# Kernel tuning notes

Measured on AMD Instinct MI355X. Metric: run time of the kernel, lower is better.

Reference implementation:

```python
import jax, jax.numpy as jnp
import numpy as np

B = 2048          # batch
K = 32            # max active features per side
NF = 22528        # feature_set.num_features
L1 = 2048
L2 = 16
L3 = 32
P = 8             # num_psqt_buckets
NLS = 8           # num_ls_buckets
QP = 255.0        # 8-bit unsigned LSQ upper bound


def setup_inputs() -> dict:
    key = jax.random.key(0)
    ks = jax.random.split(key, 16)
    us = jax.random.bernoulli(ks[0], 0.5, (B, 1)).astype(jnp.float32)
    them = 1.0 - us
    white_indices = jax.random.randint(ks[1], (B, K), 0, NF)
    black_indices = jax.random.randint(ks[2], (B, K), 0, NF)
    white_values = jnp.ones((B, K), jnp.float32)
    black_values = jnp.ones((B, K), jnp.float32)
    psqt_indices = jax.random.randint(ks[3], (B,), 0, P)
    layer_stack_indices = jax.random.randint(ks[4], (B,), 0, NLS)
    # parameters
    ft_weight = jax.random.normal(ks[5], (NF, L1 + P), jnp.float32) * 0.01
    ft_bias = jax.random.normal(ks[6], (L1 + P,), jnp.float32) * 0.01
    lsq_s = jnp.full((4,), 1.0 / 128.0, jnp.float32)  # per-group step size
    W1 = jax.random.normal(ks[7], (NLS, L2, L1), jnp.float32) * (1.0 / np.sqrt(L1))
    b1 = jnp.zeros((NLS, L2), jnp.float32)
    W2 = jax.random.normal(ks[8], (NLS, L3, L2), jnp.float32) * (1.0 / np.sqrt(L2))
    b2 = jnp.zeros((NLS, L3), jnp.float32)
    Wo = jax.random.normal(ks[9], (NLS, 1, L3), jnp.float32) * (1.0 / np.sqrt(L3))
    bo = jnp.zeros((NLS, 1), jnp.float32)
    return dict(us=us, them=them, white_indices=white_indices, white_values=white_values,
                black_indices=black_indices, black_values=black_values,
                psqt_indices=psqt_indices, layer_stack_indices=layer_stack_indices,
                ft_weight=ft_weight, ft_bias=ft_bias, lsq_s=lsq_s,
                W1=W1, b1=b1, W2=W2, b2=b2, Wo=Wo, bo=bo)


def _feature_transform(idx, val, ft_weight, ft_bias):
    # sparse accumulation: sum_k val[b,k] * ft_weight[idx[b,k], :]
    emb = ft_weight[idx]                           # [B, K, L1+P]
    return jnp.einsum('bk,bkd->bd', val, emb) + ft_bias


def _lsq(x, s):
    # LSQ activation, 4 groups over feature dim, 8-bit unsigned, STE round
    b, d = x.shape
    g = x.reshape(b, 4, d // 4) / s[None, :, None]
    gc = jnp.clip(g, 0.0, QP)
    gq = gc + jax.lax.stop_gradient(jnp.round(gc) - gc)
    return (gq * s[None, :, None]).reshape(b, d)


def reference(us, them, white_indices, white_values, black_indices, black_values,
              psqt_indices, layer_stack_indices,
              ft_weight, ft_bias, lsq_s, W1, b1, W2, b2, Wo, bo):
    wp = _feature_transform(white_indices, white_values, ft_weight, ft_bias)
    bp = _feature_transform(black_indices, black_values, ft_weight, ft_bias)
    w, wpsqt = wp[:, :L1], wp[:, L1:]
    b, bpsqt = bp[:, :L1], bp[:, L1:]
    l0 = us * jnp.concatenate([w, b], axis=1) + them * jnp.concatenate([b, w], axis=1)
    l0q = _lsq(l0, lsq_s)                          # [B, 2*L1]
    s0, s1, s2, s3 = jnp.split(l0q, 4, axis=1)
    l0_mixed = jnp.concatenate([s0 * s1, s2 * s3], axis=1)   # [B, L1]
    # psqt bucket gather
    wps = jnp.take_along_axis(wpsqt, psqt_indices[:, None], axis=1)  # [B,1]
    bps = jnp.take_along_axis(bpsqt, psqt_indices[:, None], axis=1)
    # per-sample layer-stack (expert) selection
    i = layer_stack_indices
    h1 = jnp.clip(jnp.einsum('bi,boi->bo', l0_mixed, W1[i]) + b1[i], 0.0, 1.0)
    h2 = jnp.clip(jnp.einsum('bi,boi->bo', h1, W2[i]) + b2[i], 0.0, 1.0)
    ls_out = jnp.einsum('bi,boi->bo', h2, Wo[i]) + bo[i]     # [B,1]
    return ls_out + (wps - bps) * (us - 0.5)
```

## Files before the change

kernel.cpp:

```cpp
#include <hip/hip_runtime.h>

#define BB 2048
#define K 32
#define ROW 2056
#define L1D 2048
#define NFEAT 22528

typedef unsigned short us8 __attribute__((ext_vector_type(8)));
typedef float f8 __attribute__((ext_vector_type(8)));

#define TBLC_BYTES ((size_t)NFEAT * 2048 * 2)
#define W1_ELEMS   ((size_t)8 * 16 * L1D)
#define W1_OFF     TBLC_BYTES
#define WS_NEEDED  (TBLC_BYTES + W1_ELEMS * 2)

#define TBL_N8 (NFEAT * 256)
#define W1_N8  (W1_ELEMS / 8)

__device__ __forceinline__ float bf2f(unsigned short s) {
    union { unsigned int u; float f; } v; v.u = ((unsigned int)s) << 16; return v.f;
}

__device__ __forceinline__ unsigned short f2bf(float f) {
    union { float f; unsigned int u; } v; v.f = f;
    const unsigned int u = v.u;
    return (unsigned short)((u + 0x7fffu + ((u >> 16) & 1u)) >> 16);
}

__device__ __forceinline__ void fma4(float4& a, float v, const float4 t) {
    a.x = fmaf(v, t.x, a.x); a.y = fmaf(v, t.y, a.y);
    a.z = fmaf(v, t.z, a.z); a.w = fmaf(v, t.w, a.w);
}

__device__ __forceinline__ float4 add4(float4 a, float4 b) {
    float4 r; r.x = a.x + b.x; r.y = a.y + b.y; r.z = a.z + b.z; r.w = a.w + b.w;
    return r;
}

__device__ __forceinline__ float4 mix4(float ua, float4 a, float ub, float4 b) {
    float4 r;
    r.x = fmaf(ua, a.x, ub * b.x); r.y = fmaf(ua, a.y, ub * b.y);
    r.z = fmaf(ua, a.z, ub * b.z); r.w = fmaf(ua, a.w, ub * b.w);
    return r;
}

__device__ __forceinline__ float lsq1(float g, float s) {
    return rintf(fminf(fmaxf(g / s, 0.f), 255.f)) * s;
}

__device__ __forceinline__ float4 lsq4(float4 g, float s) {
    float4 r;
    r.x = lsq1(g.x, s); r.y = lsq1(g.y, s); r.z = lsq1(g.z, s); r.w = lsq1(g.w, s);
    return r;
}

__device__ __forceinline__ float4 mul4(float4 a, float4 b) {
    float4 r; r.x = a.x * b.x; r.y = a.y * b.y; r.z = a.z * b.z; r.w = a.w * b.w;
    return r;
}

__global__ __launch_bounds__(256) void conv_all(const float* __restrict__ ftw,
                                                const float* __restrict__ W1,
                                                unsigned short* __restrict__ tblc,
                                                unsigned short* __restrict__ w1bf) {
    int i = blockIdx.x * 256 + threadIdx.x;
    const int stride = gridDim.x * 256;
    for (; i < TBL_N8 + W1_N8; i += stride) {
        const float* src;
        unsigned short* dst;
        if (i < TBL_N8) {
            const int row = i >> 8, c = i & 255;
            src = ftw + (size_t)row * ROW + c * 8;
            dst = tblc + ((size_t)row << 11) + c * 8;
        } else {
            const int j = i - TBL_N8;
            src = W1 + (size_t)j * 8;
            dst = w1bf + (size_t)j * 8;
        }
        const float4 a = ((const float4*)src)[0];
        const float4 b = ((const float4*)src)[1];
        us8 o;
        o[0] = f2bf(a.x); o[1] = f2bf(a.y); o[2] = f2bf(a.z); o[3] = f2bf(a.w);
        o[4] = f2bf(b.x); o[5] = f2bf(b.y); o[6] = f2bf(b.z); o[7] = f2bf(b.w);
        *(us8*)dst = o;
    }
}

__global__ __launch_bounds__(256, 8) void nnue_main(
    const float* __restrict__ us_p, const float* __restrict__ them_p,
    const int* __restrict__ widx, const float* __restrict__ wval,
    const int* __restrict__ bidx, const float* __restrict__ bval,
    const int* __restrict__ psqt_idx, const int* __restrict__ ls_idx,
    const float* __restrict__ ftw,
    const float* __restrict__ ftb, const float* __restrict__ lsq_s,
    const unsigned short* __restrict__ tblc,
    const unsigned short* __restrict__ w1bf,
    const float* __restrict__ b1, const float* __restrict__ W2,
    const float* __restrict__ b2, const float* __restrict__ Wo,
    const float* __restrict__ bo, float* __restrict__ out)
{
    const int b = blockIdx.x;
    const int t = threadIdx.x;

    __shared__ f8    sQA[256];
    __shared__ f8    sQB[256];
    __shared__ float sH1t[16];
    __shared__ float sH1[16];
    __shared__ float sH2[32];
    __shared__ float sPsq;

    const float usv = us_p[b];
    const float thv = them_p[b];

    f8 aw = (f8)0.f, ab = (f8)0.f;
    #pragma unroll 8
    for (int k = 0; k < K; ++k) {
        const int   iw = widx[b * K + k];
        const float vw = wval[b * K + k];
        const int   ib = bidx[b * K + k];
        const float vb = bval[b * K + k];
        const us8 lw = ((const us8*)(tblc + ((size_t)iw << 11)))[t];
        const us8 lb = ((const us8*)(tblc + ((size_t)ib << 11)))[t];
        #pragma unroll
        for (int j = 0; j < 8; ++j) aw[j] = fmaf(vw, bf2f(lw[j]), aw[j]);
        #pragma unroll
        for (int j = 0; j < 8; ++j) ab[j] = fmaf(vb, bf2f(lb[j]), ab[j]);
    }

    const int pi = psqt_idx[b];
    if (t < 64) {
        const int k = t & 31;
        const int   idx = (t < 32) ? widx[b * K + k] : bidx[b * K + k];
        const float val = (t < 32) ? wval[b * K + k] : bval[b * K + k];
        float c = val * ftw[(size_t)idx * ROW + 2048 + pi];
        c += __shfl_down(c, 16, 32); c += __shfl_down(c, 8, 32);
        c += __shfl_down(c, 4, 32);  c += __shfl_down(c, 2, 32);
        c += __shfl_down(c, 1, 32);
        const float bsum = __shfl(c, 32);
        if (t == 0) sPsq = (c - bsum) * (usv - 0.5f);
    }

    const float s0 = lsq_s[0], s1 = lsq_s[1], s2 = lsq_s[2], s3 = lsq_s[3];
    const float4 bl = ((const float4*)ftb)[2 * t];
    const float4 bh = ((const float4*)ftb)[2 * t + 1];
    float4 awl = {aw[0], aw[1], aw[2], aw[3]}, awh = {aw[4], aw[5], aw[6], aw[7]};
    float4 abl = {ab[0], ab[1], ab[2], ab[3]}, abh = {ab[4], ab[5], ab[6], ab[7]};
    awl = add4(awl, bl); awh = add4(awh, bh);
    abl = add4(abl, bl); abh = add4(abh, bh);
    const float sA = (t < 128) ? s0 : s1;
    const float sB = (t < 128) ? s2 : s3;
    const float4 qal = lsq4(mix4(usv, awl, thv, abl), sA);
    const float4 qah = lsq4(mix4(usv, awh, thv, abh), sA);
    const float4 qbl = lsq4(mix4(usv, abl, thv, awl), sB);
    const float4 qbh = lsq4(mix4(usv, abh, thv, awh), sB);
    f8 qa, qb;
    qa[0]=qal.x; qa[1]=qal.y; qa[2]=qal.z; qa[3]=qal.w;
    qa[4]=qah.x; qa[5]=qah.y; qa[6]=qah.z; qa[7]=qah.w;
    qb[0]=qbl.x; qb[1]=qbl.y; qb[2]=qbl.z; qb[3]=qbl.w;
    qb[4]=qbh.x; qb[5]=qbh.y; qb[6]=qbh.z; qb[7]=qbh.w;
    sQA[t] = qa;
    sQB[t] = qb;
    __syncthreads();

    if (t < 128) {
        const f8 m = sQA[t] * sQA[t + 128];
        sQA[t] = m;
    } else {
        const f8 m = sQB[t - 128] * sQB[t];
        sQB[t] = m;
    }
    __syncthreads();

    const int i = ls_idx[b];
    {
        const int o   = t >> 4;
        const int sub = t & 15;
        const us8* Wrow = (const us8*)(w1bf + (((size_t)i * 16 + o) << 11));
        f8 a8 = (f8)0.f;
        #pragma unroll
        for (int jj = 0; jj < 8; ++jj) {
            const int c = sub + (jj << 4);
            const f8 m = sQA[c];
            const us8 w = Wrow[c];
            #pragma unroll
            for (int j = 0; j < 8; ++j) a8[j] = fmaf(m[j], bf2f(w[j]), a8[j]);
        }
        #pragma unroll
        for (int jj = 8; jj < 16; ++jj) {
            const int c = sub + (jj << 4);
            const f8 m = sQB[c];
            const us8 w = Wrow[c];
            #pragma unroll
            for (int j = 0; j < 8; ++j) a8[j] = fmaf(m[j], bf2f(w[j]), a8[j]);
        }
        float acc = ((a8[0]+a8[1]) + (a8[2]+a8[3])) + ((a8[4]+a8[5]) + (a8[6]+a8[7]));
        acc += __shfl_down(acc, 8, 16); acc += __shfl_down(acc, 4, 16);
        acc += __shfl_down(acc, 2, 16); acc += __shfl_down(acc, 1, 16);
        if (sub == 0) sH1t[o] = acc;
    }
    __syncthreads();

    if (t < 16) {
        const float v = sH1t[t] + b1[i * 16 + t];
        sH1[t] = fminf(fmaxf(v, 0.f), 1.f);
    }
    __syncthreads();

    if (t < 32) {
        const float* W2i = W2 + (size_t)i * 32 * 16 + t * 16;
        float v = b2[i * 32 + t];
        #pragma unroll
        for (int j = 0; j < 16; ++j) v = fmaf(sH1[j], W2i[j], v);
        sH2[t] = fminf(fmaxf(v, 0.f), 1.f);
    }
    __syncthreads();

    if (t == 0) {
        const float* Woi = Wo + (size_t)i * 32;
        float v = bo[i];
        #pragma unroll
        for (int j = 0; j < 32; ++j) v = fmaf(sH2[j], Woi[j], v);
        out[b] = v + sPsq;
    }
}

__global__ __launch_bounds__(512, 8) void nnue_fwd_f32(
    const float* __restrict__ us_p, const float* __restrict__ them_p,
    const int* __restrict__ widx, const float* __restrict__ wval,
    const int* __restrict__ bidx, const float* __restrict__ bval,
    const int* __restrict__ psqt_idx, const int* __restrict__ ls_idx,
    const float* __restrict__ ftw, const float* __restrict__ ftb,
    const float* __restrict__ lsq_s, const float* __restrict__ W1,
    const float* __restrict__ b1, const float* __restrict__ W2,
    const float* __restrict__ b2, const float* __restrict__ Wo,
    const float* __restrict__ bo, float* __restrict__ out)
{
    const int b = blockIdx.x;
    const int t = threadIdx.x;
    __shared__ float4 sQA[512]; __shared__ float4 sQB[512]; __shared__ float4 sM[512];
    __shared__ float sH1t[16]; __shared__ float sH1[16]; __shared__ float sH2[32];
    __shared__ float sPsq;
    const float usv = us_p[b]; const float thv = them_p[b];
    float4 aw = {0,0,0,0}, ab = {0,0,0,0};
    #pragma unroll 4
    for (int k = 0; k < K; ++k) {
        const int iw = widx[b*K+k]; const float vw = wval[b*K+k];
        const int ib = bidx[b*K+k]; const float vb = bval[b*K+k];
        fma4(aw, vw, ((const float4*)(ftw + (size_t)iw * ROW))[t]);
        fma4(ab, vb, ((const float4*)(ftw + (size_t)ib * ROW))[t]);
    }
    const int pi = psqt_idx[b];
    if (t < 64) {
        const int k = t & 31;
        const int   idx = (t < 32) ? widx[b*K+k] : bidx[b*K+k];
        const float val = (t < 32) ? wval[b*K+k] : bval[b*K+k];
        float c = val * ftw[(size_t)idx * ROW + 2048 + pi];
        c += __shfl_down(c, 16, 32); c += __shfl_down(c, 8, 32);
        c += __shfl_down(c, 4, 32); c += __shfl_down(c, 2, 32); c += __shfl_down(c, 1, 32);
        const float bsum = __shfl(c, 32);
        if (t == 0) sPsq = (c - bsum) * (usv - 0.5f);
    }
    const float s0 = lsq_s[0], s1 = lsq_s[1], s2 = lsq_s[2], s3 = lsq_s[3];
    const float4 bias = ((const float4*)ftb)[t];
    aw = add4(aw, bias); ab = add4(ab, bias);
    const float sA = (t < 256) ? s0 : s1;
    const float sB = (t < 256) ? s2 : s3;
    sQA[t] = lsq4(mix4(usv, aw, thv, ab), sA);
    sQB[t] = lsq4(mix4(usv, ab, thv, aw), sB);
    __syncthreads();
    if (t < 256) { sM[t] = mul4(sQA[t], sQA[t+256]); sM[t+256] = mul4(sQB[t], sQB[t+256]); }
    __syncthreads();
    const int i = ls_idx[b];
    const float* W1i = W1 + (size_t)i * 16 * L1D;
    {
        const int o = t >> 5; const int sub = t & 31;
        const float4* Wrow = (const float4*)(W1i + o * L1D);
        float4 a4 = {0,0,0,0};
        #pragma unroll
        for (int jj = 0; jj < 16; ++jj) {
            const int j4 = sub + (jj << 5);
            const float4 m = sM[j4]; const float4 w = Wrow[j4];
            a4.x = fmaf(m.x, w.x, a4.x); a4.y = fmaf(m.y, w.y, a4.y);
            a4.z = fmaf(m.z, w.z, a4.z); a4.w = fmaf(m.w, w.w, a4.w);
        }
        float acc = (a4.x + a4.y) + (a4.z + a4.w);
        acc += __shfl_down(acc, 16, 32); acc += __shfl_down(acc, 8, 32);
        acc += __shfl_down(acc, 4, 32); acc += __shfl_down(acc, 2, 32); acc += __shfl_down(acc, 1, 32);
        if (sub == 0) sH1t[o] = acc;
    }
    __syncthreads();
    if (t < 16) sH1[t] = fminf(fmaxf(sH1t[t] + b1[i*16+t], 0.f), 1.f);
    __syncthreads();
    if (t < 32) {
        const float* W2i = W2 + (size_t)i * 32 * 16 + t * 16;
        float v = b2[i*32+t];
        #pragma unroll
        for (int j = 0; j < 16; ++j) v = fmaf(sH1[j], W2i[j], v);
        sH2[t] = fminf(fmaxf(v, 0.f), 1.f);
    }
    __syncthreads();
    if (t == 0) {
        const float* Woi = Wo + (size_t)i * 32;
        float v = bo[i];
        #pragma unroll
        for (int j = 0; j < 32; ++j) v = fmaf(sH2[j], Woi[j], v);
        out[b] = v + sPsq;
    }
}

extern "C" void kernel_launch(void* const* d_in, const int* in_sizes, int n_in,
                              void* d_out, int out_size, void* d_ws, size_t ws_size,
                              hipStream_t stream) {
    const float* us_p  = (const float*)d_in[0];
    const float* them  = (const float*)d_in[1];
    const int*   widx  = (const int*)d_in[2];
    const float* wval  = (const float*)d_in[3];
    const int*   bidx  = (const int*)d_in[4];
    const float* bval  = (const float*)d_in[5];
    const int*   pidx  = (const int*)d_in[6];
    const int*   lidx  = (const int*)d_in[7];
    const float* ftw   = (const float*)d_in[8];
    const float* ftb   = (const float*)d_in[9];
    const float* lsqs  = (const float*)d_in[10];
    const float* W1    = (const float*)d_in[11];
    const float* b1    = (const float*)d_in[12];
    const float* W2    = (const float*)d_in[13];
    const float* b2    = (const float*)d_in[14];
    const float* Wo    = (const float*)d_in[15];
    const float* bo    = (const float*)d_in[16];
    float* out = (float*)d_out;

    if (ws_size >= WS_NEEDED) {
        unsigned short* tblc = (unsigned short*)d_ws;
        unsigned short* w1bf = (unsigned short*)((char*)d_ws + W1_OFF);
        conv_all<<<dim3(8192), dim3(256), 0, stream>>>(ftw, W1, tblc, w1bf);
        nnue_main<<<dim3(BB), dim3(256), 0, stream>>>(
            us_p, them, widx, wval, bidx, bval, pidx, lidx,
            ftw, ftb, lsqs, tblc, w1bf, b1, W2, b2, Wo, bo, out);
    } else {
        nnue_fwd_f32<<<dim3(BB), dim3(512), 0, stream>>>(
            us_p, them, widx, wval, bidx, bval, pidx, lidx,
            ftw, ftb, lsqs, W1, b1, W2, b2, Wo, bo, out);
    }
}
```

Before: 378.6 us.

## Slice feature table into column blocks and split gather from layer stack

The bf16 feature table is re-laid out into 32 column slices of 64 values per row, so each gather block reads a small, cache-resident slice for a group of 32 samples. A new gather_mix kernel accumulates, applies bias and LSQ, forms the pairwise product and writes a bf16 mixed activation buffer G. A separate combine kernel then runs the layer stack from G. The aim is better L2 reuse of table rows across samples. The cost is an extra kernel launch, a round trip through global memory for G, and bf16 rounding of the mixed activations.

```diff
diff --git a/kernel.cpp b/kernel.cpp
--- a/kernel.cpp
+++ b/kernel.cpp
@@ -5,17 +5,20 @@
 #define ROW 2056
 #define L1D 2048
 #define NFEAT 22528
+#define NSL 32
 
 typedef unsigned short us8 __attribute__((ext_vector_type(8)));
 typedef float f8 __attribute__((ext_vector_type(8)));
 
-#define TBLC_BYTES ((size_t)NFEAT * 2048 * 2)
+#define TBL2_BYTES ((size_t)NSL * NFEAT * 64 * 2)
 #define W1_ELEMS   ((size_t)8 * 16 * L1D)
-#define W1_OFF     TBLC_BYTES
-#define WS_NEEDED  (TBLC_BYTES + W1_ELEMS * 2)
-
-#define TBL_N8 (NFEAT * 256)
-#define W1_N8  (W1_ELEMS / 8)
+#define W1_OFF     TBL2_BYTES
+#define G_OFF      (TBL2_BYTES + W1_ELEMS * 2)
+#define G_BYTES    ((size_t)BB * L1D * 2)
+#define WS_NEEDED  (G_OFF + G_BYTES)
+
+#define TBL2_N8 (NSL * NFEAT * 8)
+#define W1_N8   ((int)(W1_ELEMS / 8))
 
 __device__ __forceinline__ float bf2f(unsigned short s) {
     union { unsigned int u; float f; } v; v.u = ((unsigned int)s) << 16; return v.f;
@@ -61,39 +64,134 @@
 
 __global__ __launch_bounds__(256) void conv_all(const float* __restrict__ ftw,
                                                 const float* __restrict__ W1,
-                                                unsigned short* __restrict__ tblc,
+                                                unsigned short* __restrict__ tbl2,
                                                 unsigned short* __restrict__ w1bf) {
     int i = blockIdx.x * 256 + threadIdx.x;
     const int stride = gridDim.x * 256;
-    for (; i < TBL_N8 + W1_N8; i += stride) {
+    for (; i < TBL2_N8 + W1_N8; i += stride) {
         const float* src;
         unsigned short* dst;
-        if (i < TBL_N8) {
-            const int row = i >> 8, c = i & 255;
-            src = ftw + (size_t)row * ROW + c * 8;
-            dst = tblc + ((size_t)row << 11) + c * 8;
+        if (i < TBL2_N8) {
+            const int s   = i / (NFEAT * 8);
+            const int rem = i - s * (NFEAT * 8);
+            const int r = rem >> 3, o = rem & 7;
+            const int col = (o < 4) ? (s * 32 + o * 8) : (1024 + s * 32 + (o - 4) * 8);
+            src = ftw + (size_t)r * ROW + col;
+            dst = tbl2 + (size_t)i * 8;
         } else {
-            const int j = i - TBL_N8;
+            const int j = i - TBL2_N8;
             src = W1 + (size_t)j * 8;
             dst = w1bf + (size_t)j * 8;
         }
         const float4 a = ((const float4*)src)[0];
         const float4 b = ((const float4*)src)[1];
-        us8 o;
-        o[0] = f2bf(a.x); o[1] = f2bf(a.y); o[2] = f2bf(a.z); o[3] = f2bf(a.w);
-        o[4] = f2bf(b.x); o[5] = f2bf(b.y); o[6] = f2bf(b.z); o[7] = f2bf(b.w);
-        *(us8*)dst = o;
-    }
-}
-
-__global__ __launch_bounds__(256, 8) void nnue_main(
+        us8 o8;
+        o8[0] = f2bf(a.x); o8[1] = f2bf(a.y); o8[2] = f2bf(a.z); o8[3] = f2bf(a.w);
+        o8[4] = f2bf(b.x); o8[5] = f2bf(b.y); o8[6] = f2bf(b.z); o8[7] = f2bf(b.w);
+        *(us8*)dst = o8;
+    }
+}
+
+__global__ __launch_bounds__(512, 8) void gather_mix(
     const float* __restrict__ us_p, const float* __restrict__ them_p,
+    const int* __restrict__ widx, const float* __restrict__ wval,
+    const int* __restrict__ bidx, const float* __restrict__ bval,
+    const float* __restrict__ ftb, const float* __restrict__ lsq_s,
+    const unsigned short* __restrict__ tbl2,
+    unsigned short* __restrict__ G)
+{
+    __shared__ char smemA[16384];
+    __shared__ f8 sQm[256];
+    __shared__ f8 sQs[256];
+    int*   sI  = (int*)smemA;
+    float* sV  = (float*)(smemA + 8192);
+    f8*    sEx = (f8*)smemA;
+
+    const int blk = blockIdx.x;
+    const int p = blk >> 8, r = blk & 255;
+    const int slice = (r & 7) + 8 * (p >> 1);
+    const int group = (r >> 3) + 32 * (p & 1);
+    const int t = threadIdx.x;
+
+    const int base = group * 1024;
+    sI[t]        = widx[base + t];        sI[512 + t]  = widx[base + 512 + t];
+    sI[1024 + t] = bidx[base + t];        sI[1536 + t] = bidx[base + 512 + t];
+    sV[t]        = wval[base + t];        sV[512 + t]  = wval[base + 512 + t];
+    sV[1024 + t] = bval[base + t];        sV[1536 + t] = bval[base + 512 + t];
+    __syncthreads();
+
+    const int sl    = t >> 4;
+    const int c     = t & 15;
+    const int persp = c >> 3;
+    const int ho    = c & 7;
+    const int half  = ho >> 2;
+    const int oct   = ho & 3;
+    const int sample = group * 32 + sl;
+
+    const float usv = us_p[sample];
+    const float thv = them_p[sample];
+    const float sm  = half ? lsq_s[1] : lsq_s[0];
+    const float ss  = half ? lsq_s[3] : lsq_s[2];
+
+    const unsigned short* tb = tbl2 + (size_t)slice * NFEAT * 64 + half * 32 + oct * 8;
+    const int ib = persp * 1024 + sl * 32;
+    f8 acc = (f8)0.f;
+    #pragma unroll 8
+    for (int k = 0; k < 32; ++k) {
+        const int   idx = sI[ib + k];
+        const float v   = sV[ib + k];
+        const us8 L = *(const us8*)(tb + (size_t)idx * 64);
+        #pragma unroll
+        for (int j = 0; j < 8; ++j) acc[j] = fmaf(v, bf2f(L[j]), acc[j]);
+    }
+
+    const int colc = half * 1024 + slice * 32 + oct * 8;
+    {
+        const float4 b0 = ((const float4*)(ftb + colc))[0];
+        const float4 b1v = ((const float4*)(ftb + colc))[1];
+        acc[0] += b0.x;  acc[1] += b0.y;  acc[2] += b0.z;  acc[3] += b0.w;
+        acc[4] += b1v.x; acc[5] += b1v.y; acc[6] += b1v.z; acc[7] += b1v.w;
+    }
+
+    __syncthreads();
+    sEx[t] = acc;
+    __syncthreads();
+
+    if (persp == 0) {
+        const f8 w8 = sEx[t];
+        const f8 b8 = sEx[t + 8];
+        f8 qm, qs;
+        #pragma unroll
+        for (int j = 0; j < 8; ++j) {
+            qm[j] = lsq1(fmaf(usv, w8[j], thv * b8[j]), sm);
+            qs[j] = lsq1(fmaf(usv, b8[j], thv * w8[j]), ss);
+        }
+        const int q = sl * 8 + ho;
+        sQm[q] = qm;
+        sQs[q] = qs;
+    }
+    __syncthreads();
+
+    if (t < 128) {
+        const int sl2 = t >> 2, o2 = t & 3;
+        const f8 mlo = sQm[sl2 * 8 + o2] * sQm[sl2 * 8 + 4 + o2];
+        const f8 mhi = sQs[sl2 * 8 + o2] * sQs[sl2 * 8 + 4 + o2];
+        us8 alo, ahi;
+        #pragma unroll
+        for (int j = 0; j < 8; ++j) { alo[j] = f2bf(mlo[j]); ahi[j] = f2bf(mhi[j]); }
+        unsigned short* gp = G + (size_t)(group * 32 + sl2) * 2048;
+        *(us8*)(gp + slice * 32 + o2 * 8)        = alo;
+        *(us8*)(gp + 1024 + slice * 32 + o2 * 8) = ahi;
+    }
+}
+
+__global__ __launch_bounds__(256, 8) void combine(
+    const float* __restrict__ us_p,
     const int* __restrict__ widx, const float* __restrict__ wval,
     const int* __restrict__ bidx, const float* __restrict__ bval,
     const int* __restrict__ psqt_idx, const int* __restrict__ ls_idx,
     const float* __restrict__ ftw,
-    const float* __restrict__ ftb, const float* __restrict__ lsq_s,
-    const unsigned short* __restrict__ tblc,
+    const unsigned short* __restrict__ G,
     const unsigned short* __restrict__ w1bf,
     const float* __restrict__ b1, const float* __restrict__ W2,
     const float* __restrict__ b2, const float* __restrict__ Wo,
@@ -102,29 +200,20 @@
     const int b = blockIdx.x;
     const int t = threadIdx.x;
 
-    __shared__ f8    sQA[256];
-    __shared__ f8    sQB[256];
+    __shared__ f8    sM[256];
     __shared__ float sH1t[16];
     __shared__ float sH1[16];
     __shared__ float sH2[32];
     __shared__ float sPsq;
 
     const float usv = us_p[b];
-    const float thv = them_p[b];
-
-    f8 aw = (f8)0.f, ab = (f8)0.f;
-    #pragma unroll 8
-    for (int k = 0; k < K; ++k) {
-        const int   iw = widx[b * K + k];
-        const float vw = wval[b * K + k];
-        const int   ib = bidx[b * K + k];
-        const float vb = bval[b * K + k];
-        const us8 lw = ((const us8*)(tblc + ((size_t)iw << 11)))[t];
-        const us8 lb = ((const us8*)(tblc + ((size_t)ib << 11)))[t];
-        #pragma unroll
-        for (int j = 0; j < 8; ++j) aw[j] = fmaf(vw, bf2f(lw[j]), aw[j]);
-        #pragma unroll
-        for (int j = 0; j < 8; ++j) ab[j] = fmaf(vb, bf2f(lb[j]), ab[j]);
+
+    {
+        const us8 mu = ((const us8*)(G + (size_t)b * 2048))[t];
+        f8 mf;
+        #pragma unroll
+        for (int j = 0; j < 8; ++j) mf[j] = bf2f(mu[j]);
+        sM[t] = mf;
     }
 
     const int pi = psqt_idx[b];
@@ -132,42 +221,12 @@
         const int k = t & 31;
         const int   idx = (t < 32) ? widx[b * K + k] : bidx[b * K + k];
         const float val = (t < 32) ? wval[b * K + k] : bval[b * K + k];
-        float c = val * ftw[(size_t)idx * ROW + 2048 + pi];
-        c += __shfl_down(c, 16, 32); c += __shfl_down(c, 8, 32);
-        c += __shfl_down(c, 4, 32);  c += __shfl_down(c, 2, 32);
-        c += __shfl_down(c, 1, 32);
-        const float bsum = __shfl(c, 32);
-        if (t == 0) sPsq = (c - bsum) * (usv - 0.5f);
-    }
-
-    const float s0 = lsq_s[0], s1 = lsq_s[1], s2 = lsq_s[2], s3 = lsq_s[3];
-    const float4 bl = ((const float4*)ftb)[2 * t];
-    const float4 bh = ((const float4*)ftb)[2 * t + 1];
-    float4 awl = {aw[0], aw[1], aw[2], aw[3]}, awh = {aw[4], aw[5], aw[6], aw[7]};
-    float4 abl = {ab[0], ab[1], ab[2], ab[3]}, abh = {ab[4], ab[5], ab[6], ab[7]};
-    awl = add4(awl, bl); awh = add4(awh, bh);
-    abl = add4(abl, bl); abh = add4(abh, bh);
-    const float sA = (t < 128) ? s0 : s1;
-    const float sB = (t < 128) ? s2 : s3;
-    const float4 qal = lsq4(mix4(usv, awl, thv, abl), sA);
-    const float4 qah = lsq4(mix4(usv, awh, thv, abh), sA);
-    const float4 qbl = lsq4(mix4(usv, abl, thv, awl), sB);
-    const float4 qbh = lsq4(mix4(usv, abh, thv, awh), sB);
-    f8 qa, qb;
-    qa[0]=qal.x; qa[1]=qal.y; qa[2]=qal.z; qa[3]=qal.w;
-    qa[4]=qah.x; qa[5]=qah.y; qa[6]=qah.z; qa[7]=qah.w;
-    qb[0]=qbl.x; qb[1]=qbl.y; qb[2]=qbl.z; qb[3]=qbl.w;
-    qb[4]=qbh.x; qb[5]=qbh.y; qb[6]=qbh.z; qb[7]=qbh.w;
-    sQA[t] = qa;
-    sQB[t] = qb;
-    __syncthreads();
-
-    if (t < 128) {
-        const f8 m = sQA[t] * sQA[t + 128];
-        sQA[t] = m;
-    } else {
-        const f8 m = sQB[t - 128] * sQB[t];
-        sQB[t] = m;
+        float cc = val * ftw[(size_t)idx * ROW + 2048 + pi];
+        cc += __shfl_down(cc, 16, 32); cc += __shfl_down(cc, 8, 32);
+        cc += __shfl_down(cc, 4, 32);  cc += __shfl_down(cc, 2, 32);
+        cc += __shfl_down(cc, 1, 32);
+        const float bsum = __shfl(cc, 32);
+        if (t == 0) sPsq = (cc - bsum) * (usv - 0.5f);
     }
     __syncthreads();
 
@@ -178,18 +237,10 @@
         const us8* Wrow = (const us8*)(w1bf + (((size_t)i * 16 + o) << 11));
         f8 a8 = (f8)0.f;
         #pragma unroll
-        for (int jj = 0; jj < 8; ++jj) {
-            const int c = sub + (jj << 4);
-            const f8 m = sQA[c];
-            const us8 w = Wrow[c];
-            #pragma unroll
-            for (int j = 0; j < 8; ++j) a8[j] = fmaf(m[j], bf2f(w[j]), a8[j]);
-        }
-        #pragma unroll
-        for (int jj = 8; jj < 16; ++jj) {
-            const int c = sub + (jj << 4);
-            const f8 m = sQB[c];
-            const us8 w = Wrow[c];
+        for (int jj = 0; jj < 16; ++jj) {
+            const int cidx = sub + (jj << 4);
+            const f8 m = sM[cidx];
+            const us8 w = Wrow[cidx];
             #pragma unroll
             for (int j = 0; j < 8; ++j) a8[j] = fmaf(m[j], bf2f(w[j]), a8[j]);
         }
@@ -237,7 +288,7 @@
 {
     const int b = blockIdx.x;
     const int t = threadIdx.x;
-    __shared__ float4 sQA[512]; __shared__ float4 sQB[512]; __shared__ float4 sM[512];
+    __shared__ float4 sQA[512]; __shared__ float4 sQB[512]; __shared__ float4 sMx[512];
     __shared__ float sH1t[16]; __shared__ float sH1[16]; __shared__ float sH2[32];
     __shared__ float sPsq;
     const float usv = us_p[b]; const float thv = them_p[b];
@@ -245,20 +296,20 @@
     #pragma unroll 4
     for (int k = 0; k < K; ++k) {
         const int iw = widx[b*K+k]; const float vw = wval[b*K+k];
-        const int ib = bidx[b*K+k]; const float vb = bval[b*K+k];
+        const int ibx = bidx[b*K+k]; const float vb = bval[b*K+k];
         fma4(aw, vw, ((const float4*)(ftw + (size_t)iw * ROW))[t]);
-        fma4(ab, vb, ((const float4*)(ftw + (size_t)ib * ROW))[t]);
+        fma4(ab, vb, ((const float4*)(ftw + (size_t)ibx * ROW))[t]);
     }
     const int pi = psqt_idx[b];
     if (t < 64) {
         const int k = t & 31;
         const int   idx = (t < 32) ? widx[b*K+k] : bidx[b*K+k];
         const float val = (t < 32) ? wval[b*K+k] : bval[b*K+k];
-        float c = val * ftw[(size_t)idx * ROW + 2048 + pi];
-        c += __shfl_down(c, 16, 32); c += __shfl_down(c, 8, 32);
-        c += __shfl_down(c, 4, 32); c += __shfl_down(c, 2, 32); c += __shfl_down(c, 1, 32);
-        const float bsum = __shfl(c, 32);
-        if (t == 0) sPsq = (c - bsum) * (usv - 0.5f);
+        float cc = val * ftw[(size_t)idx * ROW + 2048 + pi];
+        cc += __shfl_down(cc, 16, 32); cc += __shfl_down(cc, 8, 32);
+        cc += __shfl_down(cc, 4, 32); cc += __shfl_down(cc, 2, 32); cc += __shfl_down(cc, 1, 32);
+        const float bsum = __shfl(cc, 32);
+        if (t == 0) sPsq = (cc - bsum) * (usv - 0.5f);
     }
     const float s0 = lsq_s[0], s1 = lsq_s[1], s2 = lsq_s[2], s3 = lsq_s[3];
     const float4 bias = ((const float4*)ftb)[t];
@@ -268,7 +319,7 @@
     sQA[t] = lsq4(mix4(usv, aw, thv, ab), sA);
     sQB[t] = lsq4(mix4(usv, ab, thv, aw), sB);
     __syncthreads();
-    if (t < 256) { sM[t] = mul4(sQA[t], sQA[t+256]); sM[t+256] = mul4(sQB[t], sQB[t+256]); }
+    if (t < 256) { sMx[t] = mul4(sQA[t], sQA[t+256]); sMx[t+256] = mul4(sQB[t], sQB[t+256]); }
     __syncthreads();
     const int i = ls_idx[b];
     const float* W1i = W1 + (size_t)i * 16 * L1D;
@@ -279,7 +330,7 @@
         #pragma unroll
         for (int jj = 0; jj < 16; ++jj) {
             const int j4 = sub + (jj << 5);
-            const float4 m = sM[j4]; const float4 w = Wrow[j4];
+            const float4 m = sMx[j4]; const float4 w = Wrow[j4];
             a4.x = fmaf(m.x, w.x, a4.x); a4.y = fmaf(m.y, w.y, a4.y);
             a4.z = fmaf(m.z, w.z, a4.z); a4.w = fmaf(m.w, w.w, a4.w);
         }
@@ -331,12 +382,15 @@
     float* out = (float*)d_out;
 
     if (ws_size >= WS_NEEDED) {
-        unsigned short* tblc = (unsigned short*)d_ws;
+        unsigned short* tbl2 = (unsigned short*)d_ws;
         unsigned short* w1bf = (unsigned short*)((char*)d_ws + W1_OFF);
-        conv_all<<<dim3(8192), dim3(256), 0, stream>>>(ftw, W1, tblc, w1bf);
-        nnue_main<<<dim3(BB), dim3(256), 0, stream>>>(
-            us_p, them, widx, wval, bidx, bval, pidx, lidx,
-            ftw, ftb, lsqs, tblc, w1bf, b1, W2, b2, Wo, bo, out);
+        unsigned short* G    = (unsigned short*)((char*)d_ws + G_OFF);
+        conv_all<<<dim3(8192), dim3(256), 0, stream>>>(ftw, W1, tbl2, w1bf);
+        gather_mix<<<dim3(2048), dim3(512), 0, stream>>>(
+            us_p, them, widx, wval, bidx, bval, ftb, lsqs, tbl2, G);
+        combine<<<dim3(BB), dim3(256), 0, stream>>>(
+            us_p, widx, wval, bidx, bval, pidx, lidx,
+            ftw, G, w1bf, b1, W2, b2, Wo, bo, out);
     } else {
         nnue_fwd_f32<<<dim3(BB), dim3(512), 0, stream>>>(
             us_p, them, widx, wval, bidx, bval, pidx, lidx,
```

Result: no change. 371.6 us (-1.8%).
